# Kernel optimization log

Measured on AMD Instinct MI355X. Metric: run time of the kernel, lower is better.

## Reference

```python
import jax, jax.numpy as jnp
import numpy as np


def setup_inputs() -> dict:
    key = jax.random.key(0)
    k1, k2, k3, k4 = jax.random.split(key, 4)
    B, H, L, D = 2, 16, 2048, 64
    q = jax.random.normal(k1, (B, H, L, D), dtype=jnp.float32)
    k = jax.random.normal(k2, (B, H, L, D), dtype=jnp.float32)
    v = jax.random.normal(k3, (B, H, L, D), dtype=jnp.float32)
    mask = jax.random.randint(k4, (B, 1, L, L), 0, 2, dtype=jnp.int32)
    return {"q": q, "k": k, "v": v, "mask": mask}


def reference(q, k, v, mask):
    d_tensor = q.shape[-1]
    # NegativeReLU: pass through only negative values and 0
    v_neg = -jax.nn.relu(-v)
    # score: [B,H,L,L]
    score = jnp.einsum("bhqd,bhkd->bhqk", q, k) / jnp.sqrt(
        jnp.asarray(d_tensor, dtype=q.dtype))
    score = jnp.where(mask == 0, jnp.asarray(-10000.0, dtype=score.dtype), score)
    attn = jax.nn.softmax(score, axis=-1)
    return jnp.einsum("bhqk,bhkd->bhqd", attn, v_neg)
```

## Files before the change

kernel.cpp:

```cpp
#include <hip/hip_runtime.h>
#include <math.h>

typedef __bf16 bf16_t;
typedef bf16_t bf16x8 __attribute__((ext_vector_type(8)));
typedef float  f32x16 __attribute__((ext_vector_type(16)));
typedef float  f32x4  __attribute__((ext_vector_type(4)));

#define MFMA32(a, b, c) __builtin_amdgcn_mfma_f32_32x32x16_bf16((a), (b), (c), 0, 0, 0)

static __device__ __forceinline__ unsigned pk_bf16(float a, float b) {
  union { bf16_t h[2]; unsigned u; } t;
  t.h[0] = (bf16_t)a;
  t.h[1] = (bf16_t)b;
  return t.u;
}

static __device__ __forceinline__ int bit_smear(unsigned w, int pos) {
#if __has_builtin(__builtin_amdgcn_sbfe)
  return __builtin_amdgcn_sbfe((int)w, pos, 1);
#else
  return ((int)(w << (31 - pos))) >> 31;
#endif
}

__global__ __launch_bounds__(256) void prepass3(
    const float* __restrict__ kp, const float* __restrict__ vp,
    const int* __restrict__ maskp, bf16_t* __restrict__ kfr,
    bf16_t* __restrict__ vfr, unsigned* __restrict__ mq) {
  const int bx  = blockIdx.x;
  const int tid = threadIdx.x;

  if (bx < 2048) {
    const size_t t = (size_t)bx * 256 + tid;
    const int ln = t & 63, dc = (t >> 6) & 3;
    const int kh = (t >> 8) & 63, bh = (int)(t >> 14);
    const float* s = kp + ((size_t)(bh * 2048 + kh * 32 + (ln & 31))) * 64 +
                     dc * 16 + (ln >> 5) * 8;
    f32x4 a0 = *(const f32x4*)s;
    f32x4 a1 = *(const f32x4*)(s + 4);
    bf16x8 w;
#pragma unroll
    for (int j = 0; j < 4; ++j) { w[j] = (bf16_t)a0[j]; w[4 + j] = (bf16_t)a1[j]; }
    *(bf16x8*)(kfr + t * 8) = w;
  } else if (bx < 4096) {
    const size_t t = (size_t)(bx - 2048) * 256 + tid;
    const int ln = t & 63, rr = (t >> 6) & 1, kc = (t >> 7) & 1;
    const int p = (t >> 8) & 1, kt = (t >> 9) & 31, bh = (int)(t >> 14);
    const int d    = rr * 32 + (ln & 31);
    const int hh   = ln >> 5;
    const int kb   = kt * 64 + p * 32 + kc * 16;
    const float* s = vp + ((size_t)(bh * 2048 + kb)) * 64 + d;
    bf16_t w[8];
#pragma unroll
    for (int j = 0; j < 8; ++j) {
      const int key = hh * 4 + (j & 3) + 8 * (j >> 2);
      w[j] = (bf16_t)fminf(s[(size_t)key * 64], 0.f);
    }
    *(bf16x8*)(vfr + t * 8) = *(bf16x8*)w;
  } else {
    const unsigned gt = (unsigned)(bx - 4096) * 256u + (unsigned)tid;
    const int q  = gt & 2047;
    const int p  = (gt >> 11) & 1;
    const int it = (gt >> 12) & 31;
    const int b  = (int)(gt >> 17);
    const int* mr = maskp + ((size_t)b * 2048 + q) * 2048 + it * 64 + p * 32;
    int m[32];
#pragma unroll
    for (int i = 0; i < 8; ++i) {
      const int4 a = *(const int4*)(mr + i * 4);
      m[i * 4 + 0] = a.x; m[i * 4 + 1] = a.y;
      m[i * 4 + 2] = a.z; m[i * 4 + 3] = a.w;
    }
    unsigned w = 0;
#pragma unroll
    for (int j = 0; j < 32; ++j) {
      const int koff = (j & 3) + 8 * ((j >> 2) & 3) + 4 * (j >> 4);
      if (m[koff] == 0) w |= (1u << j);
    }
    mq[((size_t)(b * 32 + it) * 2 + p) * 2048 + q] = w;
  }
}

__global__ __launch_bounds__(256, 4) void nrev_attn_ws3(
    const float* __restrict__ qp, const bf16_t* __restrict__ kfr,
    const bf16_t* __restrict__ vfr, const unsigned* __restrict__ mq,
    float* __restrict__ outp) {
  constexpr int L = 2048, D = 64;
  __shared__ float Oe[2][64][68];
  __shared__ float lsum[2][2][32];

  const int tid  = threadIdx.x;
  const int lane = tid & 63;
  const int wv   = tid >> 6;
  const int p    = wv >> 1;
  const int g    = wv & 1;
  const int col  = lane & 31;
  const int hh   = lane >> 5;
  const int hsh  = hh << 4;
  const int blk  = blockIdx.x;
  const int bh   = (blk & 7) * 4 + (blk >> 8);
  const int qt   = (blk >> 3) & 31;
  const int bb   = bh >> 4;
  const int q0   = qt * 64;
  const float c1 = 0.18033688011112042f;

  bf16x8 qf[4];
  {
    const float* gq = qp + (size_t)(bh * L + q0 + g * 32 + col) * D;
#pragma unroll
    for (int dc = 0; dc < 4; ++dc) {
      const float* ptr = gq + dc * 16 + hh * 8;
      f32x4 f0 = *(const f32x4*)ptr;
      f32x4 f1 = *(const f32x4*)(ptr + 4);
      bf16x8 t;
#pragma unroll
      for (int j = 0; j < 4; ++j) {
        t[j]     = (bf16_t)(f0[j] * c1);
        t[4 + j] = (bf16_t)(f1[j] * c1);
      }
      qf[dc] = t;
    }
  }

  const char* kpt = (const char*)kfr + (size_t)bh * 262144 + p * 4096 + (size_t)lane * 16;
  const char* vpt = (const char*)vfr + (size_t)bh * 262144 + p * 4096 + (size_t)lane * 16;
  const int   qq  = q0 + g * 32 + col;
  const unsigned* mpt = mq + ((size_t)bb * 64 + p) * 2048 + qq;

  union { unsigned u[4]; bf16x8 v; } onesu;
  onesu.u[0] = onesu.u[1] = onesu.u[2] = onesu.u[3] = 0x3F803F80u;
  const bf16x8 onesv = onesu.v;

  f32x16 acc0, acc1, accL;
#pragma unroll
  for (int i = 0; i < 16; ++i) { acc0[i] = 0.f; acc1[i] = 0.f; accL[i] = 0.f; }

  bf16x8 kf0 = *(const bf16x8*)(kpt + 0);
  bf16x8 kf1 = *(const bf16x8*)(kpt + 1024);
  bf16x8 kf2 = *(const bf16x8*)(kpt + 2048);
  bf16x8 kf3 = *(const bf16x8*)(kpt + 3072);
  unsigned bitsw = mpt[0];

  for (int it = 0; it < 32; ++it) {
    const int itn = (it < 31) ? it + 1 : 31;
    const char* kn = kpt + (size_t)itn * 8192;
    bf16x8 kn0 = *(const bf16x8*)(kn + 0);
    bf16x8 kn1 = *(const bf16x8*)(kn + 1024);
    bf16x8 kn2 = *(const bf16x8*)(kn + 2048);
    bf16x8 kn3 = *(const bf16x8*)(kn + 3072);
    const unsigned bw_n = mpt[(size_t)itn * 4096];
    const char* vg = vpt + (size_t)it * 8192;
    bf16x8 vf0 = *(const bf16x8*)(vg + 0);
    bf16x8 vf1 = *(const bf16x8*)(vg + 1024);
    bf16x8 vf2 = *(const bf16x8*)(vg + 2048);
    bf16x8 vf3 = *(const bf16x8*)(vg + 3072);

    const unsigned wsh = bitsw >> hsh;
    f32x16 st0;
#pragma unroll
    for (int r = 0; r < 16; ++r)
      st0[r] = __uint_as_float((unsigned)bit_smear(wsh, r) & 0xC6800000u);

    st0 = MFMA32(kf0, qf[0], st0);
    st0 = MFMA32(kf1, qf[1], st0);
    st0 = MFMA32(kf2, qf[2], st0);
    st0 = MFMA32(kf3, qf[3], st0);

#pragma unroll
    for (int r = 0; r < 16; ++r) st0[r] = __builtin_amdgcn_exp2f(st0[r]);

    union { unsigned u[4]; bf16x8 v; } b0;
    b0.u[0] = pk_bf16(st0[0], st0[1]);
    b0.u[1] = pk_bf16(st0[2], st0[3]);
    b0.u[2] = pk_bf16(st0[4], st0[5]);
    b0.u[3] = pk_bf16(st0[6], st0[7]);
    acc0 = MFMA32(vf0, b0.v, acc0);
    acc1 = MFMA32(vf1, b0.v, acc1);
    accL = MFMA32(onesv, b0.v, accL);

    union { unsigned u[4]; bf16x8 v; } b1;
    b1.u[0] = pk_bf16(st0[8],  st0[9]);
    b1.u[1] = pk_bf16(st0[10], st0[11]);
    b1.u[2] = pk_bf16(st0[12], st0[13]);
    b1.u[3] = pk_bf16(st0[14], st0[15]);
    acc0 = MFMA32(vf2, b1.v, acc0);
    acc1 = MFMA32(vf3, b1.v, acc1);
    accL = MFMA32(onesv, b1.v, accL);

    kf0 = kn0; kf1 = kn1; kf2 = kn2; kf3 = kn3;
    bitsw = bw_n;
  }

  if (hh == 0) lsum[g][p][col] = accL[0];
  __syncthreads();
  const float scale = 1.f / (lsum[g][0][col] + lsum[g][1][col]);

#pragma unroll
  for (int dt = 0; dt < 2; ++dt)
#pragma unroll
    for (int g2 = 0; g2 < 4; ++g2) {
      f32x4 w;
#pragma unroll
      for (int j = 0; j < 4; ++j)
        w[j] = (dt ? acc1[g2 * 4 + j] : acc0[g2 * 4 + j]) * scale;
      *(f32x4*)&Oe[p][g * 32 + col][g2 * 8 + hh * 4 + dt * 32] = w;
    }
  __syncthreads();
#pragma unroll
  for (int i = 0; i < 4; ++i) {
    const int idx = tid + i * 256;
    const int row = idx >> 4, c4 = idx & 15;
    f32x4 v0 = *(const f32x4*)&Oe[0][row][c4 * 4];
    f32x4 v1 = *(const f32x4*)&Oe[1][row][c4 * 4];
    f32x4 vs = v0 + v1;
    *(f32x4*)&outp[(size_t)(bh * L + q0 + row) * D + c4 * 4] = vs;
  }
}

__global__ __launch_bounds__(256, 4) void nrev_attn_fb(
    const float* __restrict__ qp, const float* __restrict__ kp,
    const float* __restrict__ vp, const int* __restrict__ maskp,
    float* __restrict__ outp) {
  constexpr int L = 2048, D = 64;
  __shared__ union alignas(16) SMem {
    struct {
      bf16_t K[64 * 72];
      bf16_t V[64 * 72];
      unsigned long long mb[64];
    } s;
    float Oe[2][64][68];
  } sm;
  __shared__ float mlbuf[2][2][32][2];

  const int tid  = threadIdx.x;
  const int lane = tid & 63;
  const int wv   = tid >> 6;
  const int p    = wv >> 1;
  const int g    = wv & 1;
  const int col  = lane & 31;
  const int hh   = lane >> 5;
  const int blk  = blockIdx.x;
  const int bh   = (blk & 7) * 4 + (blk >> 8);
  const int qt   = (blk >> 3) & 31;
  const int bb   = bh >> 4;
  const int q0   = qt * 64;
  const float c1 = 0.18033688011112042f;

  bf16x8 qf[4];
  {
    const float* gq = qp + (size_t)(bh * L + q0 + g * 32 + col) * D;
#pragma unroll
    for (int dc = 0; dc < 4; ++dc) {
      const float* ptr = gq + dc * 16 + hh * 8;
      f32x4 f0 = *(const f32x4*)ptr;
      f32x4 f1 = *(const f32x4*)(ptr + 4);
      bf16x8 t;
#pragma unroll
      for (int j = 0; j < 4; ++j) {
        t[j]     = (bf16_t)(f0[j] * c1);
        t[4 + j] = (bf16_t)(f1[j] * c1);
      }
      qf[dc] = t;
    }
  }

  f32x16 acc0, acc1;
#pragma unroll
  for (int i = 0; i < 16; ++i) { acc0[i] = 0.f; acc1[i] = 0.f; }
  float m_run = -__builtin_inff();
  float l_run = 0.f;

  for (int kt = 0; kt < L; kt += 64) {
    __syncthreads();
    {
      const int key = tid >> 2, dp = tid & 3;
      const float* gk = kp + (size_t)(bh * L + kt + key) * D + dp * 16;
      f32x4 a0 = *(const f32x4*)gk;
      f32x4 a1 = *(const f32x4*)(gk + 4);
      f32x4 a2 = *(const f32x4*)(gk + 8);
      f32x4 a3 = *(const f32x4*)(gk + 12);
      bf16x8 w0, w1;
#pragma unroll
      for (int j = 0; j < 4; ++j) {
        w0[j] = (bf16_t)a0[j]; w0[4 + j] = (bf16_t)a1[j];
        w1[j] = (bf16_t)a2[j]; w1[4 + j] = (bf16_t)a3[j];
      }
      *(bf16x8*)&sm.s.K[key * 72 + dp * 16]     = w0;
      *(bf16x8*)&sm.s.K[key * 72 + dp * 16 + 8] = w1;
    }
    {
      const int w16 = wv * 16;
      const float* gv = vp + (size_t)(bh * L + kt + w16) * D + lane;
      bf16x8 w0, w1;
#pragma unroll
      for (int i = 0; i < 8; ++i) {
        w0[i] = (bf16_t)fminf(gv[(size_t)i * D], 0.f);
        w1[i] = (bf16_t)fminf(gv[(size_t)(i + 8) * D], 0.f);
      }
      *(bf16x8*)&sm.s.V[lane * 72 + w16]     = w0;
      *(bf16x8*)&sm.s.V[lane * 72 + w16 + 8] = w1;
    }
    for (int i = 0; i < 16; ++i) {
      const int row = wv * 16 + i;
      int mv = maskp[(size_t)bb * L * L + (size_t)(q0 + row) * L + kt + lane];
      unsigned long long bal = __ballot(mv != 0);
      if (lane == 0) sm.s.mb[row] = bal;
    }
    __syncthreads();

    f32x16 st0;
#pragma unroll
    for (int i = 0; i < 16; ++i) st0[i] = 0.f;
#pragma unroll
    for (int dc = 0; dc < 4; ++dc) {
      bf16x8 a0 = *(const bf16x8*)&sm.s.K[(p * 32 + col) * 72 + dc * 16 + hh * 8];
      st0 = MFMA32(a0, qf[dc], st0);
    }

    float M = st0[0];
#pragma unroll
    for (int r = 1; r < 16; ++r) M = fmaxf(M, st0[r]);
#pragma unroll
    for (int sh = 1; sh < 64; sh <<= 1) M = fmaxf(M, __shfl_xor(M, sh));
    if (M > m_run) {
      const float alpha = exp2f(m_run - M);
      l_run *= alpha;
#pragma unroll
      for (int r = 0; r < 16; ++r) { acc0[r] *= alpha; acc1[r] *= alpha; }
      m_run = M;
    }

    const unsigned long long bits = sm.s.mb[g * 32 + col];
    const unsigned kb = ((unsigned)(bits >> (32 * p))) >> (4 * hh);
    float Sl = 0.f;
#pragma unroll
    for (int r = 0; r < 16; ++r) {
      const int c = (r & 3) + 8 * (r >> 2);
      float p0 = exp2f(st0[r] - m_run);
      p0 = ((kb >> c) & 1u) ? p0 : 0.f;
      st0[r] = p0;
      Sl += p0;
    }
    Sl += __shfl_xor(Sl, 32);
    l_run += Sl;

#pragma unroll
    for (int kc = 0; kc < 2; ++kc) {
      const unsigned pk0  = pk_bf16(st0[8 * kc + 0], st0[8 * kc + 1]);
      const unsigned pk0b = pk_bf16(st0[8 * kc + 2], st0[8 * kc + 3]);
      const unsigned pk1  = pk_bf16(st0[8 * kc + 4], st0[8 * kc + 5]);
      const unsigned pk1b = pk_bf16(st0[8 * kc + 6], st0[8 * kc + 7]);
      const unsigned sh0  = __shfl_xor(pk0, 32);
      const unsigned sh0b = __shfl_xor(pk0b, 32);
      const unsigned sh1  = __shfl_xor(pk1, 32);
      const unsigned sh1b = __shfl_xor(pk1b, 32);
      union { unsigned u[4]; bf16x8 v; } bbv;
      bbv.u[0] = hh ? sh1  : pk0;
      bbv.u[1] = hh ? sh1b : pk0b;
      bbv.u[2] = hh ? pk1  : sh0;
      bbv.u[3] = hh ? pk1b : sh0b;
      const int kbase = p * 32 + kc * 16 + hh * 8;
      bf16x8 av0 = *(const bf16x8*)&sm.s.V[col * 72        + kbase];
      bf16x8 av1 = *(const bf16x8*)&sm.s.V[(col + 32) * 72 + kbase];
      acc0 = MFMA32(av0, bbv.v, acc0);
      acc1 = MFMA32(av1, bbv.v, acc1);
    }
  }

  if (hh == 0) {
    mlbuf[g][p][col][0] = m_run;
    mlbuf[g][p][col][1] = l_run;
  }
  __syncthreads();
  const float m0 = mlbuf[g][0][col][0], l0v = mlbuf[g][0][col][1];
  const float m1 = mlbuf[g][1][col][0], l1v = mlbuf[g][1][col][1];
  const float ms = fmaxf(m0, m1);
  const float a0s = exp2f(m0 - ms), a1s = exp2f(m1 - ms);
  const float lst = a0s * l0v + a1s * l1v;
  const float scale = (p ? a1s : a0s) / lst;

#pragma unroll
  for (int dt = 0; dt < 2; ++dt)
#pragma unroll
    for (int g2 = 0; g2 < 4; ++g2) {
      f32x4 w;
#pragma unroll
      for (int j = 0; j < 4; ++j)
        w[j] = (dt ? acc1[g2 * 4 + j] : acc0[g2 * 4 + j]) * scale;
      *(f32x4*)&sm.Oe[p][g * 32 + col][g2 * 8 + hh * 4 + dt * 32] = w;
    }
  __syncthreads();
#pragma unroll
  for (int i = 0; i < 4; ++i) {
    const int idx = tid + i * 256;
    const int row = idx >> 4, c4 = idx & 15;
    f32x4 v0 = *(const f32x4*)&sm.Oe[0][row][c4 * 4];
    f32x4 v1 = *(const f32x4*)&sm.Oe[1][row][c4 * 4];
    f32x4 vs = v0 + v1;
    *(f32x4*)&outp[(size_t)(bh * L + q0 + row) * D + c4 * 4] = vs;
  }
}

extern "C" void kernel_launch(void* const* d_in, const int* in_sizes, int n_in,
                              void* d_out, int out_size, void* d_ws, size_t ws_size,
                              hipStream_t stream) {
  (void)in_sizes; (void)n_in; (void)out_size;
  const float* qp = (const float*)d_in[0];
  const float* kp = (const float*)d_in[1];
  const float* vp = (const float*)d_in[2];
  const int*   mp = (const int*)d_in[3];
  float* op = (float*)d_out;

  const size_t kOff = 0;
  const size_t vOff = (size_t)8 * 1024 * 1024;
  const size_t mOff = (size_t)16 * 1024 * 1024;
  const size_t need = mOff + (size_t)1024 * 1024;

  if (d_ws != nullptr && ws_size >= need) {
    bf16_t* kb = (bf16_t*)((char*)d_ws + kOff);
    bf16_t* vt = (bf16_t*)((char*)d_ws + vOff);
    unsigned* mqp = (unsigned*)((char*)d_ws + mOff);
    hipLaunchKernelGGL(prepass3, dim3(5120), dim3(256), 0, stream,
                       kp, vp, mp, kb, vt, mqp);
    hipLaunchKernelGGL(nrev_attn_ws3, dim3(1024), dim3(256), 0, stream,
                       qp, kb, vt, mqp, op);
  } else {
    hipLaunchKernelGGL(nrev_attn_fb, dim3(1024), dim3(256), 0, stream,
                       qp, kp, vp, mp, op);
  }
}
```

Baseline: 168.6 us.

## Split key range across four waves per 32-query tile and drop ones-MFMA row sum

The attention kernel now gives each block 32 queries instead of 64 and launches twice as many blocks. The four waves split the key dimension four ways rather than two query groups times two key halves. The softmax denominator is now accumulated with scalar adds instead of an extra MFMA against a ones vector. Partial outputs are combined through LDS in two phases, and launch bounds ask for 8 blocks per CU. This cuts MFMA work and per-thread iterations and raises occupancy. In exchange, each block repeats the Q load, adds an extra LDS reduction step and sync, and the 8-block bound puts more pressure on registers.

Measured after the change: 405.3 us. 140% more time.

```diff
diff --git a/kernel.cpp b/kernel.cpp
--- a/kernel.cpp
+++ b/kernel.cpp
@@ -81,32 +81,30 @@
   }
 }
 
-__global__ __launch_bounds__(256, 4) void nrev_attn_ws3(
+__global__ __launch_bounds__(256, 8) void nrev_attn_ws4(
     const float* __restrict__ qp, const bf16_t* __restrict__ kfr,
     const bf16_t* __restrict__ vfr, const unsigned* __restrict__ mq,
     float* __restrict__ outp) {
   constexpr int L = 2048, D = 64;
-  __shared__ float Oe[2][64][68];
-  __shared__ float lsum[2][2][32];
+  __shared__ float Oe[2][32][68];
+  __shared__ float lsum[4][2][32];
 
   const int tid  = threadIdx.x;
   const int lane = tid & 63;
   const int wv   = tid >> 6;
-  const int p    = wv >> 1;
-  const int g    = wv & 1;
   const int col  = lane & 31;
   const int hh   = lane >> 5;
   const int hsh  = hh << 4;
   const int blk  = blockIdx.x;
-  const int bh   = (blk & 7) * 4 + (blk >> 8);
-  const int qt   = (blk >> 3) & 31;
+  const int bh   = (blk & 7) * 4 + (blk >> 9);
+  const int qt   = (blk >> 3) & 63;
   const int bb   = bh >> 4;
-  const int q0   = qt * 64;
+  const int q0   = qt * 32;
   const float c1 = 0.18033688011112042f;
 
   bf16x8 qf[4];
   {
-    const float* gq = qp + (size_t)(bh * L + q0 + g * 32 + col) * D;
+    const float* gq = qp + (size_t)(bh * L + q0 + col) * D;
 #pragma unroll
     for (int dc = 0; dc < 4; ++dc) {
       const float* ptr = gq + dc * 16 + hh * 8;
@@ -122,18 +120,19 @@
     }
   }
 
-  const char* kpt = (const char*)kfr + (size_t)bh * 262144 + p * 4096 + (size_t)lane * 16;
-  const char* vpt = (const char*)vfr + (size_t)bh * 262144 + p * 4096 + (size_t)lane * 16;
-  const int   qq  = q0 + g * 32 + col;
-  const unsigned* mpt = mq + ((size_t)bb * 64 + p) * 2048 + qq;
-
-  union { unsigned u[4]; bf16x8 v; } onesu;
-  onesu.u[0] = onesu.u[1] = onesu.u[2] = onesu.u[3] = 0x3F803F80u;
-  const bf16x8 onesv = onesu.v;
-
-  f32x16 acc0, acc1, accL;
-#pragma unroll
-  for (int i = 0; i < 16; ++i) { acc0[i] = 0.f; acc1[i] = 0.f; accL[i] = 0.f; }
+  const int w2 = wv >> 1;
+  const int p  = wv & 1;
+  const char* kpt = (const char*)kfr + (size_t)bh * 262144 + w2 * 8192 +
+                    p * 4096 + (size_t)lane * 16;
+  const char* vpt = (const char*)vfr + (size_t)bh * 262144 + w2 * 8192 +
+                    p * 4096 + (size_t)lane * 16;
+  const int qq = q0 + col;
+  const unsigned* mpt = mq + ((size_t)(bb * 32 + w2) * 2 + p) * 2048 + qq;
+
+  f32x16 acc0, acc1;
+#pragma unroll
+  for (int i = 0; i < 16; ++i) { acc0[i] = 0.f; acc1[i] = 0.f; }
+  float l_run = 0.f;
 
   bf16x8 kf0 = *(const bf16x8*)(kpt + 0);
   bf16x8 kf1 = *(const bf16x8*)(kpt + 1024);
@@ -141,15 +140,15 @@
   bf16x8 kf3 = *(const bf16x8*)(kpt + 3072);
   unsigned bitsw = mpt[0];
 
-  for (int it = 0; it < 32; ++it) {
-    const int itn = (it < 31) ? it + 1 : 31;
-    const char* kn = kpt + (size_t)itn * 8192;
+  for (int it = 0; it < 16; ++it) {
+    const int itn = (it < 15) ? it + 1 : 15;
+    const char* kn = kpt + (size_t)itn * 16384;
     bf16x8 kn0 = *(const bf16x8*)(kn + 0);
     bf16x8 kn1 = *(const bf16x8*)(kn + 1024);
     bf16x8 kn2 = *(const bf16x8*)(kn + 2048);
     bf16x8 kn3 = *(const bf16x8*)(kn + 3072);
-    const unsigned bw_n = mpt[(size_t)itn * 4096];
-    const char* vg = vpt + (size_t)it * 8192;
+    const unsigned bw_n = mpt[(size_t)itn * 8192];
+    const char* vg = vpt + (size_t)it * 16384;
     bf16x8 vf0 = *(const bf16x8*)(vg + 0);
     bf16x8 vf1 = *(const bf16x8*)(vg + 1024);
     bf16x8 vf2 = *(const bf16x8*)(vg + 2048);
@@ -168,6 +167,14 @@
 
 #pragma unroll
     for (int r = 0; r < 16; ++r) st0[r] = __builtin_amdgcn_exp2f(st0[r]);
+
+    {
+      const float t0 = (st0[0] + st0[1]) + (st0[2] + st0[3]);
+      const float t1 = (st0[4] + st0[5]) + (st0[6] + st0[7]);
+      const float t2 = (st0[8] + st0[9]) + (st0[10] + st0[11]);
+      const float t3 = (st0[12] + st0[13]) + (st0[14] + st0[15]);
+      l_run += (t0 + t1) + (t2 + t3);
+    }
 
     union { unsigned u[4]; bf16x8 v; } b0;
     b0.u[0] = pk_bf16(st0[0], st0[1]);
@@ -176,7 +183,6 @@
     b0.u[3] = pk_bf16(st0[6], st0[7]);
     acc0 = MFMA32(vf0, b0.v, acc0);
     acc1 = MFMA32(vf1, b0.v, acc1);
-    accL = MFMA32(onesv, b0.v, accL);
 
     union { unsigned u[4]; bf16x8 v; } b1;
     b1.u[0] = pk_bf16(st0[8],  st0[9]);
@@ -185,29 +191,47 @@
     b1.u[3] = pk_bf16(st0[14], st0[15]);
     acc0 = MFMA32(vf2, b1.v, acc0);
     acc1 = MFMA32(vf3, b1.v, acc1);
-    accL = MFMA32(onesv, b1.v, accL);
 
     kf0 = kn0; kf1 = kn1; kf2 = kn2; kf3 = kn3;
     bitsw = bw_n;
   }
 
-  if (hh == 0) lsum[g][p][col] = accL[0];
+  lsum[wv][hh][col] = l_run;
   __syncthreads();
-  const float scale = 1.f / (lsum[g][0][col] + lsum[g][1][col]);
-
-#pragma unroll
-  for (int dt = 0; dt < 2; ++dt)
-#pragma unroll
-    for (int g2 = 0; g2 < 4; ++g2) {
-      f32x4 w;
-#pragma unroll
-      for (int j = 0; j < 4; ++j)
-        w[j] = (dt ? acc1[g2 * 4 + j] : acc0[g2 * 4 + j]) * scale;
-      *(f32x4*)&Oe[p][g * 32 + col][g2 * 8 + hh * 4 + dt * 32] = w;
-    }
+  float ls = 0.f;
+#pragma unroll
+  for (int w = 0; w < 4; ++w) ls += lsum[w][0][col] + lsum[w][1][col];
+  const float scale = 1.f / ls;
+
+  if (wv < 2) {
+#pragma unroll
+    for (int dt = 0; dt < 2; ++dt)
+#pragma unroll
+      for (int g2 = 0; g2 < 4; ++g2) {
+        f32x4 w;
+#pragma unroll
+        for (int j = 0; j < 4; ++j)
+          w[j] = (dt ? acc1[g2 * 4 + j] : acc0[g2 * 4 + j]) * scale;
+        *(f32x4*)&Oe[wv][col][g2 * 8 + hh * 4 + dt * 32] = w;
+      }
+  }
   __syncthreads();
-#pragma unroll
-  for (int i = 0; i < 4; ++i) {
+  if (wv >= 2) {
+#pragma unroll
+    for (int dt = 0; dt < 2; ++dt)
+#pragma unroll
+      for (int g2 = 0; g2 < 4; ++g2) {
+        float* dst = &Oe[wv - 2][col][g2 * 8 + hh * 4 + dt * 32];
+        f32x4 w = *(f32x4*)dst;
+#pragma unroll
+        for (int j = 0; j < 4; ++j)
+          w[j] += (dt ? acc1[g2 * 4 + j] : acc0[g2 * 4 + j]) * scale;
+        *(f32x4*)dst = w;
+      }
+  }
+  __syncthreads();
+#pragma unroll
+  for (int i = 0; i < 2; ++i) {
     const int idx = tid + i * 256;
     const int row = idx >> 4, c4 = idx & 15;
     f32x4 v0 = *(const f32x4*)&Oe[0][row][c4 * 4];
@@ -422,7 +446,7 @@
     unsigned* mqp = (unsigned*)((char*)d_ws + mOff);
     hipLaunchKernelGGL(prepass3, dim3(5120), dim3(256), 0, stream,
                        kp, vp, mp, kb, vt, mqp);
-    hipLaunchKernelGGL(nrev_attn_ws3, dim3(1024), dim3(256), 0, stream,
+    hipLaunchKernelGGL(nrev_attn_ws4, dim3(2048), dim3(256), 0, stream,
                        qp, kb, vt, mqp, op);
   } else {
     hipLaunchKernelGGL(nrev_attn_fb, dim3(1024), dim3(256), 0, stream,
```

## Software-pipeline QK^T one tile ahead and replace ones-MFMA row sum with VALU adds

Applied to the files above, without the earlier changes.

The main loop now computes the score MFMAs for tile it+1 while applying exp2, packing and the PV MFMAs to tile it. K fragments and mask bits are prefetched two tiles ahead. The row-sum MFMA against a ones vector is removed; each lane sums its exp values in fp32 and the partial sums from both half-waves are combined through shared memory. This aims to hide MFMA latency behind VALU exp work and cut a third of the PV-stage MFMAs, at the cost of more live registers, which could hurt occupancy under launch_bounds(256,4).

After: 167.5 us. About the same (-0.6%).

```diff
diff --git a/kernel.cpp b/kernel.cpp
--- a/kernel.cpp
+++ b/kernel.cpp
@@ -81,13 +81,13 @@
   }
 }
 
-__global__ __launch_bounds__(256, 4) void nrev_attn_ws3(
+__global__ __launch_bounds__(256, 4) void nrev_attn_ws5(
     const float* __restrict__ qp, const bf16_t* __restrict__ kfr,
     const bf16_t* __restrict__ vfr, const unsigned* __restrict__ mq,
     float* __restrict__ outp) {
   constexpr int L = 2048, D = 64;
   __shared__ float Oe[2][64][68];
-  __shared__ float lsum[2][2][32];
+  __shared__ float lsum[2][2][2][32];
 
   const int tid  = threadIdx.x;
   const int lane = tid & 63;
@@ -124,76 +124,97 @@
 
   const char* kpt = (const char*)kfr + (size_t)bh * 262144 + p * 4096 + (size_t)lane * 16;
   const char* vpt = (const char*)vfr + (size_t)bh * 262144 + p * 4096 + (size_t)lane * 16;
-  const int   qq  = q0 + g * 32 + col;
-  const unsigned* mpt = mq + ((size_t)bb * 64 + p) * 2048 + qq;
-
-  union { unsigned u[4]; bf16x8 v; } onesu;
-  onesu.u[0] = onesu.u[1] = onesu.u[2] = onesu.u[3] = 0x3F803F80u;
-  const bf16x8 onesv = onesu.v;
-
-  f32x16 acc0, acc1, accL;
-#pragma unroll
-  for (int i = 0; i < 16; ++i) { acc0[i] = 0.f; acc1[i] = 0.f; accL[i] = 0.f; }
-
-  bf16x8 kf0 = *(const bf16x8*)(kpt + 0);
-  bf16x8 kf1 = *(const bf16x8*)(kpt + 1024);
-  bf16x8 kf2 = *(const bf16x8*)(kpt + 2048);
-  bf16x8 kf3 = *(const bf16x8*)(kpt + 3072);
-  unsigned bitsw = mpt[0];
-
+  const unsigned* mpt = mq + ((size_t)bb * 64 + p) * 2048 + q0 + g * 32 + col;
+
+  f32x16 acc0, acc1;
+#pragma unroll
+  for (int i = 0; i < 16; ++i) { acc0[i] = 0.f; acc1[i] = 0.f; }
+  float l_run = 0.f;
+
+  f32x16 st_cur;
+  {
+    bf16x8 ka0 = *(const bf16x8*)(kpt + 0);
+    bf16x8 ka1 = *(const bf16x8*)(kpt + 1024);
+    bf16x8 ka2 = *(const bf16x8*)(kpt + 2048);
+    bf16x8 ka3 = *(const bf16x8*)(kpt + 3072);
+    const unsigned bits0 = mpt[0];
+    const unsigned wsh0  = bits0 >> hsh;
+#pragma unroll
+    for (int r = 0; r < 16; ++r)
+      st_cur[r] = __uint_as_float((unsigned)bit_smear(wsh0, r) & 0xC6800000u);
+    st_cur = MFMA32(ka0, qf[0], st_cur);
+    st_cur = MFMA32(ka1, qf[1], st_cur);
+    st_cur = MFMA32(ka2, qf[2], st_cur);
+    st_cur = MFMA32(ka3, qf[3], st_cur);
+  }
+  bf16x8 kf0 = *(const bf16x8*)(kpt + 8192 + 0);
+  bf16x8 kf1 = *(const bf16x8*)(kpt + 8192 + 1024);
+  bf16x8 kf2 = *(const bf16x8*)(kpt + 8192 + 2048);
+  bf16x8 kf3 = *(const bf16x8*)(kpt + 8192 + 3072);
+  unsigned bitsB = mpt[4096];
+
+#pragma unroll 2
   for (int it = 0; it < 32; ++it) {
-    const int itn = (it < 31) ? it + 1 : 31;
-    const char* kn = kpt + (size_t)itn * 8192;
+    const int itn2 = (it < 30) ? it + 2 : 31;
+    const char* kn = kpt + (size_t)itn2 * 8192;
     bf16x8 kn0 = *(const bf16x8*)(kn + 0);
     bf16x8 kn1 = *(const bf16x8*)(kn + 1024);
     bf16x8 kn2 = *(const bf16x8*)(kn + 2048);
     bf16x8 kn3 = *(const bf16x8*)(kn + 3072);
-    const unsigned bw_n = mpt[(size_t)itn * 4096];
+    const unsigned bitsC = mpt[(size_t)itn2 * 4096];
     const char* vg = vpt + (size_t)it * 8192;
     bf16x8 vf0 = *(const bf16x8*)(vg + 0);
     bf16x8 vf1 = *(const bf16x8*)(vg + 1024);
     bf16x8 vf2 = *(const bf16x8*)(vg + 2048);
     bf16x8 vf3 = *(const bf16x8*)(vg + 3072);
 
-    const unsigned wsh = bitsw >> hsh;
-    f32x16 st0;
-#pragma unroll
-    for (int r = 0; r < 16; ++r)
-      st0[r] = __uint_as_float((unsigned)bit_smear(wsh, r) & 0xC6800000u);
-
-    st0 = MFMA32(kf0, qf[0], st0);
-    st0 = MFMA32(kf1, qf[1], st0);
-    st0 = MFMA32(kf2, qf[2], st0);
-    st0 = MFMA32(kf3, qf[3], st0);
-
-#pragma unroll
-    for (int r = 0; r < 16; ++r) st0[r] = __builtin_amdgcn_exp2f(st0[r]);
+    f32x16 st_next;
+    {
+      const unsigned wshB = bitsB >> hsh;
+#pragma unroll
+      for (int r = 0; r < 16; ++r)
+        st_next[r] = __uint_as_float((unsigned)bit_smear(wshB, r) & 0xC6800000u);
+    }
+    st_next = MFMA32(kf0, qf[0], st_next);
+    st_next = MFMA32(kf1, qf[1], st_next);
+    st_next = MFMA32(kf2, qf[2], st_next);
+    st_next = MFMA32(kf3, qf[3], st_next);
+
+#pragma unroll
+    for (int r = 0; r < 16; ++r) st_cur[r] = __builtin_amdgcn_exp2f(st_cur[r]);
+    {
+      const float t0 = (st_cur[0] + st_cur[1]) + (st_cur[2] + st_cur[3]);
+      const float t1 = (st_cur[4] + st_cur[5]) + (st_cur[6] + st_cur[7]);
+      const float t2 = (st_cur[8] + st_cur[9]) + (st_cur[10] + st_cur[11]);
+      const float t3 = (st_cur[12] + st_cur[13]) + (st_cur[14] + st_cur[15]);
+      l_run += (t0 + t1) + (t2 + t3);
+    }
 
     union { unsigned u[4]; bf16x8 v; } b0;
-    b0.u[0] = pk_bf16(st0[0], st0[1]);
-    b0.u[1] = pk_bf16(st0[2], st0[3]);
-    b0.u[2] = pk_bf16(st0[4], st0[5]);
-    b0.u[3] = pk_bf16(st0[6], st0[7]);
+    b0.u[0] = pk_bf16(st_cur[0], st_cur[1]);
+    b0.u[1] = pk_bf16(st_cur[2], st_cur[3]);
+    b0.u[2] = pk_bf16(st_cur[4], st_cur[5]);
+    b0.u[3] = pk_bf16(st_cur[6], st_cur[7]);
     acc0 = MFMA32(vf0, b0.v, acc0);
     acc1 = MFMA32(vf1, b0.v, acc1);
-    accL = MFMA32(onesv, b0.v, accL);
 
     union { unsigned u[4]; bf16x8 v; } b1;
-    b1.u[0] = pk_bf16(st0[8],  st0[9]);
-    b1.u[1] = pk_bf16(st0[10], st0[11]);
-    b1.u[2] = pk_bf16(st0[12], st0[13]);
-    b1.u[3] = pk_bf16(st0[14], st0[15]);
+    b1.u[0] = pk_bf16(st_cur[8],  st_cur[9]);
+    b1.u[1] = pk_bf16(st_cur[10], st_cur[11]);
+    b1.u[2] = pk_bf16(st_cur[12], st_cur[13]);
+    b1.u[3] = pk_bf16(st_cur[14], st_cur[15]);
     acc0 = MFMA32(vf2, b1.v, acc0);
     acc1 = MFMA32(vf3, b1.v, acc1);
-    accL = MFMA32(onesv, b1.v, accL);
-
+
+    st_cur = st_next;
     kf0 = kn0; kf1 = kn1; kf2 = kn2; kf3 = kn3;
-    bitsw = bw_n;
-  }
-
-  if (hh == 0) lsum[g][p][col] = accL[0];
+    bitsB = bitsC;
+  }
+
+  lsum[g][p][hh][col] = l_run;
   __syncthreads();
-  const float scale = 1.f / (lsum[g][0][col] + lsum[g][1][col]);
+  const float scale = 1.f / (lsum[g][0][0][col] + lsum[g][0][1][col] +
+                             lsum[g][1][0][col] + lsum[g][1][1][col]);
 
 #pragma unroll
   for (int dt = 0; dt < 2; ++dt)
@@ -422,7 +443,7 @@
     unsigned* mqp = (unsigned*)((char*)d_ws + mOff);
     hipLaunchKernelGGL(prepass3, dim3(5120), dim3(256), 0, stream,
                        kp, vp, mp, kb, vt, mqp);
-    hipLaunchKernelGGL(nrev_attn_ws3, dim3(1024), dim3(256), 0, stream,
+    hipLaunchKernelGGL(nrev_attn_ws5, dim3(1024), dim3(256), 0, stream,
                        qp, kb, vt, mqp, op);
   } else {
     hipLaunchKernelGGL(nrev_attn_fb, dim3(1024), dim3(256), 0, stream,
```
